# Performance work log

Measured on AMD Instinct MI355X. Metric: run time of the kernel, lower is better.

The kernel has to match this reference:

```python
import jax, jax.numpy as jnp
import numpy as np

B, S, D = 16, 2048, 128
SCALE = 1.0 / float(np.sqrt(D))  # scale = 1/sqrt(dim_K) per docstring


def setup_inputs() -> dict:
    key = jax.random.key(0)
    kq, kk, kv = jax.random.split(key, 3)
    Q = jax.random.normal(kq, (B, S, D), dtype=jnp.float32)
    K = jax.random.normal(kk, (B, S, D), dtype=jnp.float32)
    V = jax.random.normal(kv, (B, S, D), dtype=jnp.float32)
    return {"Q": Q, "K": K, "V": V}


def reference(Q, K, V):
    # attention = Q @ K^T * scale  -> [B, S, S]
    attn = jnp.einsum('bqd,bkd->bqk', Q, K) * SCALE
    attn = jax.nn.softmax(attn, axis=-1)
    # context = attn @ V -> [B, S, D]
    context = jnp.einsum('bqk,bkd->bqd', attn, V)
    return context
```

## Files before the change

kernel.cpp:

```cpp
#include <hip/hip_runtime.h>
#include <hip/hip_bf16.h>


#define NB 16
#define NS 2048
#define ND 128
#define KVB 32
#define NTT (NS / KVB)
#define IMG 16384
#define QSC (0.08838834764831845f * 1.4426950408889634f)

typedef __attribute__((ext_vector_type(8))) short bf16x8;
typedef __attribute__((ext_vector_type(4))) short short4v;
typedef __attribute__((ext_vector_type(16))) float f32x16;
typedef __attribute__((ext_vector_type(4))) int int4v;

__device__ __forceinline__ short f2bf(float f) {
    unsigned u = __builtin_bit_cast(unsigned, f);
    return (short)((u + 0x7fffu + ((u >> 16) & 1u)) >> 16);
}

#if __has_builtin(__builtin_amdgcn_exp2f)
#define EXP2F(x) __builtin_amdgcn_exp2f(x)
#else
#define EXP2F(x) __expf((x) * 0.6931471805599453f)
#endif

__device__ __forceinline__ void gll16(const void* g, void* l) {
    __builtin_amdgcn_global_load_lds(
        (const __attribute__((address_space(1))) uint32_t*)g,
        (__attribute__((address_space(3))) uint32_t*)l, 16, 0, 0);
}

__global__ __launch_bounds__(256, 2)
void prep_kv(const float* __restrict__ Kg, const float* __restrict__ Vg,
             uint8_t* __restrict__ ws) {
    __shared__ __align__(16) uint8_t img[2 * IMG];
    const int tid = threadIdx.x;
    const int t = blockIdx.x, b = blockIdx.y;
    const float* Kb = Kg + ((size_t)b * NS + (size_t)t * 64) * ND;
    const float* Vb = Vg + ((size_t)b * NS + (size_t)t * 64) * ND;
#pragma unroll
    for (int it = 0; it < 8; ++it) {
        int idx = it * 256 + tid;
        int r  = idx >> 5;
        int c4 = (idx & 31) << 2;
        int sub = (r >> 5) * (2 * 8192);
        int rr = r & 31;
        float4 kvv = *(const float4*)(Kb + (size_t)r * ND + c4);
        short4v ks = { f2bf(kvv.x), f2bf(kvv.y), f2bf(kvv.z), f2bf(kvv.w) };
        *(short4v*)&img[sub + rr * 256 + ((c4 * 2) ^ ((rr & 7) << 4))] = ks;
        float4 vv = *(const float4*)(Vb + (size_t)r * ND + c4);
        float vf[4] = { vv.x, vv.y, vv.z, vv.w };
#pragma unroll
        for (int di = 0; di < 4; ++di) {
            int d = c4 + di;
            *(short*)&img[sub + 8192 + d * 64 + ((rr * 2) ^ (((d >> 1) & 3) << 4))]
                = f2bf(vf[di]);
        }
    }
    __syncthreads();
    float4* dst = (float4*)(ws + (size_t)(b * (NTT / 2) + t) * (2 * IMG));
    const float4* srcl = (const float4*)img;
#pragma unroll
    for (int j = 0; j < 8; ++j)
        dst[j * 256 + tid] = srcl[j * 256 + tid];
}

__global__ __launch_bounds__(768, 3)
void sdpa_fwd(const float* __restrict__ Qg, const uint8_t* __restrict__ ws,
              float* __restrict__ Og) {
    __shared__ __align__(16) uint8_t kv[2][3][IMG];

    const int tid  = threadIdx.x;
    const int w    = tid >> 6;
    const int wq   = w & 3;
    const int wh   = w >> 2;
    const int lane = tid & 63;
    const int lr_  = lane & 31;
    const int hi   = lane >> 5;

    const int tlo  = (wh == 0) ? 0 : (22 + 21 * (wh - 1));
    const int tcnt = (wh == 0) ? 22 : 21;

    const int gid  = blockIdx.x;
    const int b    = (gid & 7) * 2 + ((gid >> 3) & 1);
    const int qblk = gid >> 4;
    const int q0w  = qblk * 128 + wq * 32;

    bf16x8 qf[8];
    {
        const float* qrow = Qg + ((size_t)b * NS + q0w + lr_) * ND;
#pragma unroll
        for (int dc = 0; dc < 8; ++dc) {
            const float4* p = (const float4*)(qrow + dc * 16 + hi * 8);
            float4 x0 = p[0], x1 = p[1];
            bf16x8 f;
            f[0] = f2bf(x0.x * QSC); f[1] = f2bf(x0.y * QSC);
            f[2] = f2bf(x0.z * QSC); f[3] = f2bf(x0.w * QSC);
            f[4] = f2bf(x1.x * QSC); f[5] = f2bf(x1.y * QSC);
            f[6] = f2bf(x1.z * QSC); f[7] = f2bf(x1.w * QSC);
            qf[dc] = f;
        }
    }

    f32x16 acc[4];
#pragma unroll
    for (int n = 0; n < 4; ++n)
#pragma unroll
        for (int r = 0; r < 16; ++r) acc[n][r] = 0.f;
    float m_run = -__builtin_inff();
    float l_run = 0.f;

    const uint8_t* wsb = ws + (size_t)b * NTT * IMG;

    auto stage = [&](int bfi, int it) {
        const uint8_t* src = wsb + (size_t)(tlo + it) * IMG
                                 + (size_t)(wq * 4096 + lane * 16);
        uint8_t* dst = &kv[bfi][wh][wq * 4096];
#pragma unroll
        for (int i = 0; i < 4; ++i)
            gll16(src + i * 1024, dst + i * 1024);
    };

    const int kbase = lr_ * 256 + ((hi * 16) ^ ((lr_ & 7) << 4));
    const int vbase = 8192 + lr_ * 64 + ((hi * 16) ^ (((lr_ >> 1) & 3) << 4));

    int buf = 0;
    stage(0, 0);
    __syncthreads();

    for (int t = 0; t < 22; ++t) {
        if (t + 1 < tcnt) stage(buf ^ 1, t + 1);

        if (t < tcnt) {
            const uint8_t* img = kv[buf][wh];

            f32x16 s0;
#pragma unroll
            for (int r = 0; r < 16; ++r) s0[r] = 0.f;
            __builtin_amdgcn_s_setprio(1);
#pragma unroll
            for (int dc = 0; dc < 8; ++dc) {
                bf16x8 k0 = *(const bf16x8*)(img + (kbase ^ (dc * 32)));
                s0 = __builtin_amdgcn_mfma_f32_32x32x16_bf16(k0, qf[dc], s0, 0, 0, 0);
            }
            __builtin_amdgcn_s_setprio(0);

            float tmax = -__builtin_inff();
#pragma unroll
            for (int r = 0; r < 16; ++r) tmax = fmaxf(tmax, s0[r]);
            float tm = fmaxf(tmax, __shfl_xor(tmax, 32));

            if (__any(tm > m_run + 8.0f)) {
                float m_new = fmaxf(m_run, tm);
                float alpha = EXP2F(m_run - m_new);
                m_run = m_new;
                l_run *= alpha;
#pragma unroll
                for (int r = 0; r < 16; ++r) {
                    float a = __shfl(alpha, (r & 3) + 8 * (r >> 2) + 4 * hi);
#pragma unroll
                    for (int n = 0; n < 4; ++n) acc[n][r] *= a;
                }
            }

            float ts = 0.f;
#pragma unroll
            for (int r = 0; r < 16; ++r) {
                s0[r] = EXP2F(s0[r] - m_run);
                ts += s0[r];
            }
            l_run += ts + __shfl_xor(ts, 32);

            int W[8];
#define PK(dst, x, y) asm("v_cvt_pk_bf16_f32 %0, %1, %2" : "=v"(dst) : "v"(x), "v"(y))
            PK(W[0], s0[0],  s0[1]);  PK(W[1], s0[2],  s0[3]);
            PK(W[2], s0[4],  s0[5]);  PK(W[3], s0[6],  s0[7]);
            PK(W[4], s0[8],  s0[9]);  PK(W[5], s0[10], s0[11]);
            PK(W[6], s0[12], s0[13]); PK(W[7], s0[14], s0[15]);
#undef PK
            bf16x8 pa[2];
#pragma unroll
            for (int g = 0; g < 2; ++g) {
                int W0 = W[g * 4 + 0], W1 = W[g * 4 + 1];
                int W2 = W[g * 4 + 2], W3 = W[g * 4 + 3];
                int X0 = __shfl_xor(W0, 32), X1 = __shfl_xor(W1, 32);
                int X2 = __shfl_xor(W2, 32), X3 = __shfl_xor(W3, 32);
                int4v A;
                A[0] = hi ? X2 : W0;
                A[1] = hi ? X3 : W1;
                A[2] = hi ? W2 : X0;
                A[3] = hi ? W3 : X1;
                pa[g] = __builtin_bit_cast(bf16x8, A);
            }

            __builtin_amdgcn_s_setprio(1);
#pragma unroll
            for (int n = 0; n < 4; ++n) {
#pragma unroll
                for (int kc = 0; kc < 2; ++kc) {
                    bf16x8 vf = *(const bf16x8*)(img + ((vbase ^ (kc * 32)) + n * 2048));
                    acc[n] = __builtin_amdgcn_mfma_f32_32x32x16_bf16(pa[kc], vf, acc[n], 0, 0, 0);
                }
            }
            __builtin_amdgcn_s_setprio(0);
        }

        __syncthreads();
        buf ^= 1;
    }

    float* scr = (float*)&kv[0][0][0];
    const int sbase = wq * 4224 + lane * 66;
#pragma unroll
    for (int rnd = 1; rnd <= 2; ++rnd) {
        __syncthreads();
        if (wh == rnd) {
#pragma unroll
            for (int n = 0; n < 4; ++n)
#pragma unroll
                for (int r = 0; r < 16; ++r) scr[sbase + n * 16 + r] = acc[n][r];
            scr[sbase + 64] = m_run;
            scr[sbase + 65] = l_run;
        }
        __syncthreads();
        if (wh == 0) {
            float m1 = scr[sbase + 64], l1 = scr[sbase + 65];
            float mm = fmaxf(m_run, m1);
            float a0 = EXP2F(m_run - mm), a1 = EXP2F(m1 - mm);
            l_run = l_run * a0 + l1 * a1;
            m_run = mm;
#pragma unroll
            for (int r = 0; r < 16; ++r) {
                int row = (r & 3) + 8 * (r >> 2) + 4 * hi;
                float f0 = __shfl(a0, row), f1 = __shfl(a1, row);
#pragma unroll
                for (int n = 0; n < 4; ++n)
                    acc[n][r] = acc[n][r] * f0 + scr[sbase + n * 16 + r] * f1;
            }
        }
    }

    if (wh == 0) {
        float* ob = Og + ((size_t)b * NS + q0w) * ND + lr_;
#pragma unroll
        for (int r = 0; r < 16; ++r) {
            int row = (r & 3) + 8 * (r >> 2) + 4 * hi;
            float li = 1.f / __shfl(l_run, row);
#pragma unroll
            for (int n = 0; n < 4; ++n)
                ob[(size_t)row * ND + n * 32] = acc[n][r] * li;
        }
    }
}

extern "C" void kernel_launch(void* const* d_in, const int* in_sizes, int n_in,
                              void* d_out, int out_size, void* d_ws, size_t ws_size,
                              hipStream_t stream) {
    const float* Q = (const float*)d_in[0];
    const float* K = (const float*)d_in[1];
    const float* V = (const float*)d_in[2];
    float* O = (float*)d_out;
    (void)in_sizes; (void)n_in; (void)out_size; (void)ws_size;
    uint8_t* ws = (uint8_t*)d_ws;
    prep_kv<<<dim3(NS / 64, NB), 256, 0, stream>>>(K, V, ws);
    sdpa_fwd<<<dim3(NB * NS / 128, 1), 768, 0, stream>>>(Q, ws, O);
}
```

Baseline: 64.36 us.

## Software-pipeline QK^T of the next tile with softmax and PV of the previous

Moves K/V staging from double to triple LDS buffering and unrolls the main loop six ways. Each step issues the QK^T MFMAs for tile p while running the softmax and PV MFMAs for tile p-1, with two rotating score registers. The aim is to overlap exponent and shuffle work with matrix work inside a wave and hide LDS load latency. The cost is more LDS per block (three buffers instead of two) and 16 more live accumulator registers, which may cause spills at 768 threads per block.

```diff
diff --git a/kernel.cpp b/kernel.cpp
--- a/kernel.cpp
+++ b/kernel.cpp
@@ -70,7 +70,7 @@
 __global__ __launch_bounds__(768, 3)
 void sdpa_fwd(const float* __restrict__ Qg, const uint8_t* __restrict__ ws,
               float* __restrict__ Og) {
-    __shared__ __align__(16) uint8_t kv[2][3][IMG];
+    __shared__ __align__(16) uint8_t kv[3][3][IMG];
 
     const int tid  = threadIdx.x;
     const int w    = tid >> 6;
@@ -114,42 +114,39 @@
 
     const uint8_t* wsb = ws + (size_t)b * NTT * IMG;
 
-    auto stage = [&](int bfi, int it) {
-        const uint8_t* src = wsb + (size_t)(tlo + it) * IMG
-                                 + (size_t)(wq * 4096 + lane * 16);
-        uint8_t* dst = &kv[bfi][wh][wq * 4096];
-#pragma unroll
-        for (int i = 0; i < 4; ++i)
-            gll16(src + i * 1024, dst + i * 1024);
-    };
-
     const int kbase = lr_ * 256 + ((hi * 16) ^ ((lr_ & 7) << 4));
     const int vbase = 8192 + lr_ * 64 + ((hi * 16) ^ (((lr_ >> 1) & 3) << 4));
 
-    int buf = 0;
-    stage(0, 0);
-    __syncthreads();
-
-    for (int t = 0; t < 22; ++t) {
-        if (t + 1 < tcnt) stage(buf ^ 1, t + 1);
-
-        if (t < tcnt) {
-            const uint8_t* img = kv[buf][wh];
-
-            f32x16 s0;
-#pragma unroll
-            for (int r = 0; r < 16; ++r) s0[r] = 0.f;
+    auto st = [&](int tt, uint8_t* dst) {
+        if (tt < tcnt) {
+            const uint8_t* src = wsb + (size_t)(tlo + tt) * IMG
+                                     + (size_t)(wq * 4096 + lane * 16);
+            gll16(src,        dst);
+            gll16(src + 1024, dst + 1024);
+            gll16(src + 2048, dst + 2048);
+            gll16(src + 3072, dst + 3072);
+        }
+    };
+
+    auto qk = [&](int p, const uint8_t* img_, f32x16& sN) {
+        if (p < tcnt) {
+#pragma unroll
+            for (int r = 0; r < 16; ++r) sN[r] = 0.f;
             __builtin_amdgcn_s_setprio(1);
 #pragma unroll
             for (int dc = 0; dc < 8; ++dc) {
-                bf16x8 k0 = *(const bf16x8*)(img + (kbase ^ (dc * 32)));
-                s0 = __builtin_amdgcn_mfma_f32_32x32x16_bf16(k0, qf[dc], s0, 0, 0, 0);
+                bf16x8 k0 = *(const bf16x8*)(img_ + (kbase ^ (dc * 32)));
+                sN = __builtin_amdgcn_mfma_f32_32x32x16_bf16(k0, qf[dc], sN, 0, 0, 0);
             }
             __builtin_amdgcn_s_setprio(0);
-
+        }
+    };
+
+    auto sm = [&](int p, const uint8_t* img_, f32x16& sP) {
+        if (p >= 0 && p < tcnt) {
             float tmax = -__builtin_inff();
 #pragma unroll
-            for (int r = 0; r < 16; ++r) tmax = fmaxf(tmax, s0[r]);
+            for (int r = 0; r < 16; ++r) tmax = fmaxf(tmax, sP[r]);
             float tm = fmaxf(tmax, __shfl_xor(tmax, 32));
 
             if (__any(tm > m_run + 8.0f)) {
@@ -168,17 +165,17 @@
             float ts = 0.f;
 #pragma unroll
             for (int r = 0; r < 16; ++r) {
-                s0[r] = EXP2F(s0[r] - m_run);
-                ts += s0[r];
+                sP[r] = EXP2F(sP[r] - m_run);
+                ts += sP[r];
             }
             l_run += ts + __shfl_xor(ts, 32);
 
             int W[8];
 #define PK(dst, x, y) asm("v_cvt_pk_bf16_f32 %0, %1, %2" : "=v"(dst) : "v"(x), "v"(y))
-            PK(W[0], s0[0],  s0[1]);  PK(W[1], s0[2],  s0[3]);
-            PK(W[2], s0[4],  s0[5]);  PK(W[3], s0[6],  s0[7]);
-            PK(W[4], s0[8],  s0[9]);  PK(W[5], s0[10], s0[11]);
-            PK(W[6], s0[12], s0[13]); PK(W[7], s0[14], s0[15]);
+            PK(W[0], sP[0],  sP[1]);  PK(W[1], sP[2],  sP[3]);
+            PK(W[2], sP[4],  sP[5]);  PK(W[3], sP[6],  sP[7]);
+            PK(W[4], sP[8],  sP[9]);  PK(W[5], sP[10], sP[11]);
+            PK(W[6], sP[12], sP[13]); PK(W[7], sP[14], sP[15]);
 #undef PK
             bf16x8 pa[2];
 #pragma unroll
@@ -200,15 +197,37 @@
             for (int n = 0; n < 4; ++n) {
 #pragma unroll
                 for (int kc = 0; kc < 2; ++kc) {
-                    bf16x8 vf = *(const bf16x8*)(img + ((vbase ^ (kc * 32)) + n * 2048));
+                    bf16x8 vf = *(const bf16x8*)(img_ + ((vbase ^ (kc * 32)) + n * 2048));
                     acc[n] = __builtin_amdgcn_mfma_f32_32x32x16_bf16(pa[kc], vf, acc[n], 0, 0, 0);
                 }
             }
             __builtin_amdgcn_s_setprio(0);
         }
-
-        __syncthreads();
-        buf ^= 1;
+    };
+
+    uint8_t* b0 = &kv[wh][0][0];
+    uint8_t* b1 = &kv[wh][1][0];
+    uint8_t* b2 = &kv[wh][2][0];
+    const int so = wq * 4096;
+
+    st(0, b0 + so);
+    __syncthreads();
+
+    f32x16 sA, sB;
+    for (int i6 = 0; i6 < 4; ++i6) {
+        const int base = i6 * 6;
+        st(base + 1, b1 + so); qk(base + 0, b0, sA); sm(base - 1, b2, sB);
+        __syncthreads();
+        st(base + 2, b2 + so); qk(base + 1, b1, sB); sm(base + 0, b0, sA);
+        __syncthreads();
+        st(base + 3, b0 + so); qk(base + 2, b2, sA); sm(base + 1, b1, sB);
+        __syncthreads();
+        st(base + 4, b1 + so); qk(base + 3, b0, sB); sm(base + 2, b2, sA);
+        __syncthreads();
+        st(base + 5, b2 + so); qk(base + 4, b1, sA); sm(base + 3, b0, sB);
+        __syncthreads();
+        st(base + 6, b0 + so); qk(base + 5, b2, sB); sm(base + 4, b1, sA);
+        __syncthreads();
     }
 
     float* scr = (float*)&kv[0][0][0];
```

Result: slower. 67.81 us (+5.4%).
